# Kernel optimization log

Hardware: AMD Instinct MI355X
Metric: run time of the kernel (lower is better)

The kernel has to match this reference:

```python
import jax, jax.numpy as jnp
import numpy as np

B, H, S, D = 2, 16, 2048, 64

def setup_inputs() -> dict:
    key = jax.random.key(0)
    kq, kk, kv = jax.random.split(key, 3)
    query = jax.random.normal(kq, (B, H, S, D), dtype=jnp.float32)
    k = jax.random.normal(kk, (B, H, S, D), dtype=jnp.float32)
    value = jax.random.normal(kv, (B, H, S, D), dtype=jnp.float32)
    return {"query": query, "key": k, "value": value}

def reference(query, key, value):
    d_k = query.shape[-1]
    scale = 1.0 / jnp.sqrt(jnp.asarray(d_k, dtype=jnp.float32))
    # scores: [B, H, S, S]
    scores = jnp.einsum('bhqd,bhkd->bhqk', query, key) * scale
    attn = jax.nn.softmax(scores, axis=-1)
    # output: [B, H, S, D]
    return jnp.einsum('bhqk,bhkd->bhqd', attn, value)
```

## Files before the change

kernel.cpp:

```cpp
#include <hip/hip_runtime.h>
#include <hip/hip_bf16.h>

#define S_LEN 2048
#define HD    64
#define BH    32
#define QB    16
#define KVB   64
#define NIT   (S_LEN / KVB)
#define ELEMS_PER_ARR (BH * S_LEN * HD)

typedef __attribute__((ext_vector_type(8))) short bf16x8;
typedef __attribute__((ext_vector_type(4))) float f32x4;

union FragU { unsigned u[4]; bf16x8 v; };

__device__ __forceinline__ unsigned cvtpk(float lo, float hi) {
  unsigned r;
  asm("v_cvt_pk_bf16_f32 %0, %1, %2" : "=v"(r) : "v"(lo), "v"(hi));
  return r;
}

__device__ __forceinline__ f32x4 mfma16(bf16x8 a, bf16x8 b, f32x4 c) {
  return __builtin_amdgcn_mfma_f32_16x16x32_bf16(a, b, c, 0, 0, 0);
}

__global__ __launch_bounds__(256) void cvt_qk(
    const float* __restrict__ Q, const float* __restrict__ K,
    unsigned short* __restrict__ Qb, unsigned short* __restrict__ Kb) {
  const int which = blockIdx.x >> 11;
  const size_t i = ((size_t)(blockIdx.x & 2047) * 256 + threadIdx.x) * 8;
  const float* src = which ? K : Q;
  unsigned short* dst = which ? Kb : Qb;
  const float sc = which ? 1.0f : (0.125f * 1.44269504088896340736f);
  float4 a = *(const float4*)(src + i);
  float4 b = *(const float4*)(src + i + 4);
  uint4 w;
  w.x = cvtpk(a.x * sc, a.y * sc);
  w.y = cvtpk(a.z * sc, a.w * sc);
  w.z = cvtpk(b.x * sc, b.y * sc);
  w.w = cvtpk(b.z * sc, b.w * sc);
  *(uint4*)(dst + i) = w;
}

__global__ __launch_bounds__(256) void transpose_v(
    const float* __restrict__ V, unsigned short* __restrict__ Vt) {
  __shared__ float T[64 * 68];
  const int tid = threadIdx.x;
  const int bh = blockIdx.x >> 5;
  const int s0 = (blockIdx.x & 31) * 64;
  const float* vb = V + ((size_t)bh * S_LEN + s0) * HD;
  {
    const int r = tid >> 4, c4 = (tid & 15) * 4;
#pragma unroll
    for (int i = 0; i < 4; ++i) {
      float4 x = *(const float4*)(vb + (size_t)(r + 16 * i) * HD + c4);
      *(float4*)&T[(r + 16 * i) * 68 + c4] = x;
    }
  }
  __syncthreads();
  const int d = tid >> 2, sc = (tid & 3) * 16;
  unsigned short* out = Vt + (size_t)bh * HD * S_LEN + (size_t)d * S_LEN + s0 + sc;
  uint4 w0, w1;
  w0.x = cvtpk(T[(sc + 0) * 68 + d], T[(sc + 1) * 68 + d]);
  w0.y = cvtpk(T[(sc + 2) * 68 + d], T[(sc + 3) * 68 + d]);
  w0.z = cvtpk(T[(sc + 4) * 68 + d], T[(sc + 5) * 68 + d]);
  w0.w = cvtpk(T[(sc + 6) * 68 + d], T[(sc + 7) * 68 + d]);
  w1.x = cvtpk(T[(sc + 8) * 68 + d], T[(sc + 9) * 68 + d]);
  w1.y = cvtpk(T[(sc + 10) * 68 + d], T[(sc + 11) * 68 + d]);
  w1.z = cvtpk(T[(sc + 12) * 68 + d], T[(sc + 13) * 68 + d]);
  w1.w = cvtpk(T[(sc + 14) * 68 + d], T[(sc + 15) * 68 + d]);
  *(uint4*)out = w0;
  *(uint4*)(out + 8) = w1;
}

__device__ __forceinline__ void redist(const f32x4& pa, const f32x4& pc,
                                       int srcA, unsigned sel, FragU& pb) {
  unsigned pk0 = cvtpk(pa[0], pc[0]);
  unsigned pk1 = cvtpk(pa[1], pc[1]);
  unsigned pk2 = cvtpk(pa[2], pc[2]);
  unsigned pk3 = cvtpk(pa[3], pc[3]);
  unsigned w0 = (unsigned)__shfl((int)pk0, srcA);
  unsigned w1 = (unsigned)__shfl((int)pk1, srcA);
  unsigned w2 = (unsigned)__shfl((int)pk2, srcA);
  unsigned w3 = (unsigned)__shfl((int)pk3, srcA);
  unsigned w4 = (unsigned)__shfl((int)pk0, srcA + 16);
  unsigned w5 = (unsigned)__shfl((int)pk1, srcA + 16);
  unsigned w6 = (unsigned)__shfl((int)pk2, srcA + 16);
  unsigned w7 = (unsigned)__shfl((int)pk3, srcA + 16);
  pb.u[0] = __builtin_amdgcn_perm(w1, w0, sel);
  pb.u[1] = __builtin_amdgcn_perm(w3, w2, sel);
  pb.u[2] = __builtin_amdgcn_perm(w5, w4, sel);
  pb.u[3] = __builtin_amdgcn_perm(w7, w6, sel);
}

__global__ __launch_bounds__(256) void sdpa_main(
    const unsigned short* __restrict__ Qb, const unsigned short* __restrict__ Kb,
    const unsigned short* __restrict__ Vt, float* __restrict__ O) {
  __shared__ __align__(16) unsigned short Klds[2][KVB * 64];
  __shared__ __align__(16) unsigned short Vlds[2][HD * KVB];

  const int tid  = threadIdx.x;
  const int lane = tid & 63;
  const int wv   = tid >> 6;
  const int g    = lane >> 4;
  const int q15  = lane & 15;
  const int q7   = q15 & 7;

  const int bh   = blockIdx.x >> 5;
  const int qblk = blockIdx.x & 31;
  const int qt   = qblk * 64 + wv * QB;

  const unsigned short* Qp = Qb + (size_t)bh * S_LEN * HD;
  const unsigned short* Kp = Kb + (size_t)bh * S_LEN * HD;
  const unsigned short* Vp = Vt + (size_t)bh * HD * S_LEN;
  float* Op = O + (size_t)bh * S_LEN * HD;

  FragU qf0, qf1;
  qf0.v = *(const bf16x8*)(Qp + (size_t)(qt + q15) * HD + 8 * g);
  qf1.v = *(const bf16x8*)(Qp + (size_t)(qt + q15) * HD + 32 + 8 * g);

  const int rk = tid >> 2;
  const int qq = (tid & 3) * 16;
  const int r7 = rk & 7;
  const int wb0 = rk * 64 + (((qq >> 3)) ^ r7) * 8;
  const int wb1 = rk * 64 + (((qq >> 3) | 1) ^ r7) * 8;

  const int      srcA = 32 * (g & 1) + q15;
  const unsigned sel  = (g >= 2) ? 0x07060302u : 0x05040100u;

  bf16x8 sK0 = *(const bf16x8*)(Kp + (size_t)rk * HD + qq);
  bf16x8 sK1 = *(const bf16x8*)(Kp + (size_t)rk * HD + qq + 8);
  bf16x8 sV0 = *(const bf16x8*)(Vp + (size_t)rk * S_LEN + qq);
  bf16x8 sV1 = *(const bf16x8*)(Vp + (size_t)rk * S_LEN + qq + 8);
  *(bf16x8*)&Klds[0][wb0] = sK0;
  *(bf16x8*)&Klds[0][wb1] = sK1;
  *(bf16x8*)&Vlds[0][wb0] = sV0;
  *(bf16x8*)&Vlds[0][wb1] = sV1;
  __syncthreads();

  f32x4 acc0 = {0.f, 0.f, 0.f, 0.f};
  f32x4 acc1 = acc0, acc2 = acc0, acc3 = acc0;
  float m = -__builtin_inff();
  float l = 0.f;
  int cur = 0;

  for (int it = 0; it < NIT; ++it) {
    const bool more = (it + 1) < NIT;
    const int ktn = (it + 1) * KVB;
    if (more) {
      sK0 = *(const bf16x8*)(Kp + (size_t)(ktn + rk) * HD + qq);
      sK1 = *(const bf16x8*)(Kp + (size_t)(ktn + rk) * HD + qq + 8);
      sV0 = *(const bf16x8*)(Vp + (size_t)rk * S_LEN + ktn + qq);
      sV1 = *(const bf16x8*)(Vp + (size_t)rk * S_LEN + ktn + qq + 8);
    }
    const bf16x8* K8 = (const bf16x8*)&Klds[cur][0];
    const bf16x8* V8 = (const bf16x8*)&Vlds[cur][0];

    f32x4 st0 = {0.f, 0.f, 0.f, 0.f}, st1 = st0, st2 = st0, st3 = st0;
    {
      bf16x8 ka, kb;
      ka = K8[(q15) * 8 + (g ^ q7)];
      kb = K8[(q15) * 8 + ((g ^ 4) ^ q7)];
      st0 = mfma16(ka, qf0.v, st0); st0 = mfma16(kb, qf1.v, st0);
      ka = K8[(16 + q15) * 8 + (g ^ q7)];
      kb = K8[(16 + q15) * 8 + ((g ^ 4) ^ q7)];
      st1 = mfma16(ka, qf0.v, st1); st1 = mfma16(kb, qf1.v, st1);
      ka = K8[(32 + q15) * 8 + (g ^ q7)];
      kb = K8[(32 + q15) * 8 + ((g ^ 4) ^ q7)];
      st2 = mfma16(ka, qf0.v, st2); st2 = mfma16(kb, qf1.v, st2);
      ka = K8[(48 + q15) * 8 + (g ^ q7)];
      kb = K8[(48 + q15) * 8 + ((g ^ 4) ^ q7)];
      st3 = mfma16(ka, qf0.v, st3); st3 = mfma16(kb, qf1.v, st3);
    }

    float tm = fmaxf(fmaxf(fmaxf(st0[0], st0[1]), fmaxf(st0[2], st0[3])),
                     fmaxf(fmaxf(st1[0], st1[1]), fmaxf(st1[2], st1[3])));
    tm = fmaxf(tm, fmaxf(fmaxf(fmaxf(st2[0], st2[1]), fmaxf(st2[2], st2[3])),
                         fmaxf(fmaxf(st3[0], st3[1]), fmaxf(st3[2], st3[3]))));
    tm = fmaxf(tm, __shfl_xor(tm, 16));
    tm = fmaxf(tm, __shfl_xor(tm, 32));
    const float mn    = fmaxf(m, tm);
    const float alpha = __builtin_amdgcn_exp2f(m - mn);
    m = mn;

    float rs = 0.f;
#pragma unroll
    for (int r = 0; r < 4; ++r) {
      st0[r] = __builtin_amdgcn_exp2f(st0[r] - mn);
      st1[r] = __builtin_amdgcn_exp2f(st1[r] - mn);
      st2[r] = __builtin_amdgcn_exp2f(st2[r] - mn);
      st3[r] = __builtin_amdgcn_exp2f(st3[r] - mn);
      rs += (st0[r] + st1[r]) + (st2[r] + st3[r]);
    }
    rs += __shfl_xor(rs, 16);
    rs += __shfl_xor(rs, 32);
    l = l * alpha + rs;
    acc0 *= alpha; acc1 *= alpha; acc2 *= alpha; acc3 *= alpha;

    FragU pb0, pb1;
    redist(st0, st1, srcA, sel, pb0);
    redist(st2, st3, srcA, sel, pb1);

    {
      bf16x8 va, vb;
      va = V8[(q15) * 8 + (g ^ q7)];
      vb = V8[(q15) * 8 + ((g ^ 4) ^ q7)];
      acc0 = mfma16(va, pb0.v, acc0); acc0 = mfma16(vb, pb1.v, acc0);
      va = V8[(16 + q15) * 8 + (g ^ q7)];
      vb = V8[(16 + q15) * 8 + ((g ^ 4) ^ q7)];
      acc1 = mfma16(va, pb0.v, acc1); acc1 = mfma16(vb, pb1.v, acc1);
      va = V8[(32 + q15) * 8 + (g ^ q7)];
      vb = V8[(32 + q15) * 8 + ((g ^ 4) ^ q7)];
      acc2 = mfma16(va, pb0.v, acc2); acc2 = mfma16(vb, pb1.v, acc2);
      va = V8[(48 + q15) * 8 + (g ^ q7)];
      vb = V8[(48 + q15) * 8 + ((g ^ 4) ^ q7)];
      acc3 = mfma16(va, pb0.v, acc3); acc3 = mfma16(vb, pb1.v, acc3);
    }

    if (more) {
      *(bf16x8*)&Klds[cur ^ 1][wb0] = sK0;
      *(bf16x8*)&Klds[cur ^ 1][wb1] = sK1;
      *(bf16x8*)&Vlds[cur ^ 1][wb0] = sV0;
      *(bf16x8*)&Vlds[cur ^ 1][wb1] = sV1;
    }
    __syncthreads();
    cur ^= 1;
  }

  const float inv = 1.0f / l;
  float* orow = Op + (size_t)(qt + q15) * HD + 4 * g;
  float4 o;
  o.x = acc0[0] * inv; o.y = acc0[1] * inv; o.z = acc0[2] * inv; o.w = acc0[3] * inv;
  *(float4*)(orow + 0) = o;
  o.x = acc1[0] * inv; o.y = acc1[1] * inv; o.z = acc1[2] * inv; o.w = acc1[3] * inv;
  *(float4*)(orow + 16) = o;
  o.x = acc2[0] * inv; o.y = acc2[1] * inv; o.z = acc2[2] * inv; o.w = acc2[3] * inv;
  *(float4*)(orow + 32) = o;
  o.x = acc3[0] * inv; o.y = acc3[1] * inv; o.z = acc3[2] * inv; o.w = acc3[3] * inv;
  *(float4*)(orow + 48) = o;
}

#define KROW 72
#define VROW 40
__global__ __launch_bounds__(256) void sdpa_fallback(
    const float* __restrict__ Q, const float* __restrict__ K,
    const float* __restrict__ V, float* __restrict__ O) {
  __shared__ __align__(16) unsigned short Klds[32 * KROW];
  __shared__ __align__(16) unsigned short Vlds[HD * VROW];
  const int tid = threadIdx.x;
  const int lane = tid & 63;
  const int wv = tid >> 6;
  const int g = lane >> 4;
  const int q15 = lane & 15;
  const int bh = blockIdx.x >> 5;
  const int qblk = blockIdx.x & 31;
  const int qt = qblk * 64 + wv * QB;
  const size_t base = (size_t)bh * S_LEN * HD;
  const float* Qp = Q + base;
  const float* Kp = K + base;
  const float* Vp = V + base;
  float* Op = O + base;
  const float qs = 0.125f * 1.44269504088896340736f;
  FragU qf0, qf1;
  {
    const float* qrow = Qp + (size_t)(qt + q15) * HD + 8 * g;
    float4 a = *(const float4*)(qrow);
    float4 b = *(const float4*)(qrow + 4);
    qf0.u[0] = cvtpk(a.x * qs, a.y * qs); qf0.u[1] = cvtpk(a.z * qs, a.w * qs);
    qf0.u[2] = cvtpk(b.x * qs, b.y * qs); qf0.u[3] = cvtpk(b.z * qs, b.w * qs);
    a = *(const float4*)(qrow + 32);
    b = *(const float4*)(qrow + 36);
    qf1.u[0] = cvtpk(a.x * qs, a.y * qs); qf1.u[1] = cvtpk(a.z * qs, a.w * qs);
    qf1.u[2] = cvtpk(b.x * qs, b.y * qs); qf1.u[3] = cvtpk(b.z * qs, b.w * qs);
  }
  f32x4 acc0 = {0.f,0.f,0.f,0.f};
  f32x4 acc1 = acc0, acc2 = acc0, acc3 = acc0;
  float m = -__builtin_inff();
  float l = 0.f;
  const int srcA = 32 * (g & 1) + q15;
  const unsigned sel = (g >= 2) ? 0x07060302u : 0x05040100u;
  const int sk = tid >> 3;
  const int sd = (tid & 7) * 8;
  const bf16x8* Kv = (const bf16x8*)Klds;
  const bf16x8* Vv = (const bf16x8*)Vlds;
  for (int kt = 0; kt < S_LEN; kt += 32) {
    __syncthreads();
    {
      const float* p = Kp + (size_t)(kt + sk) * HD + sd;
      float4 a = *(const float4*)p;
      float4 b = *(const float4*)(p + 4);
      uint4 w;
      w.x = cvtpk(a.x, a.y); w.y = cvtpk(a.z, a.w);
      w.z = cvtpk(b.x, b.y); w.w = cvtpk(b.z, b.w);
      *(uint4*)&Klds[sk * KROW + sd] = w;
    }
    {
      const float* p = Vp + (size_t)(kt + sk) * HD + sd;
      float4 a = *(const float4*)p;
      float4 b = *(const float4*)(p + 4);
      unsigned u0 = cvtpk(a.x, a.y), u1 = cvtpk(a.z, a.w);
      unsigned u2 = cvtpk(b.x, b.y), u3 = cvtpk(b.z, b.w);
      Vlds[(sd + 0) * VROW + sk] = (unsigned short)(u0 & 0xffffu);
      Vlds[(sd + 1) * VROW + sk] = (unsigned short)(u0 >> 16);
      Vlds[(sd + 2) * VROW + sk] = (unsigned short)(u1 & 0xffffu);
      Vlds[(sd + 3) * VROW + sk] = (unsigned short)(u1 >> 16);
      Vlds[(sd + 4) * VROW + sk] = (unsigned short)(u2 & 0xffffu);
      Vlds[(sd + 5) * VROW + sk] = (unsigned short)(u2 >> 16);
      Vlds[(sd + 6) * VROW + sk] = (unsigned short)(u3 & 0xffffu);
      Vlds[(sd + 7) * VROW + sk] = (unsigned short)(u3 >> 16);
    }
    __syncthreads();
    f32x4 st0 = {0.f,0.f,0.f,0.f}, st1 = st0;
    {
      bf16x8 kfa = Kv[q15 * 9 + g];
      bf16x8 kfb = Kv[q15 * 9 + 4 + g];
      st0 = mfma16(kfa, qf0.v, st0);
      st0 = mfma16(kfb, qf1.v, st0);
      bf16x8 kfc = Kv[(16 + q15) * 9 + g];
      bf16x8 kfd = Kv[(16 + q15) * 9 + 4 + g];
      st1 = mfma16(kfc, qf0.v, st1);
      st1 = mfma16(kfd, qf1.v, st1);
    }
    float tm = fmaxf(fmaxf(fmaxf(st0[0], st0[1]), fmaxf(st0[2], st0[3])),
                     fmaxf(fmaxf(st1[0], st1[1]), fmaxf(st1[2], st1[3])));
    tm = fmaxf(tm, __shfl_xor(tm, 16));
    tm = fmaxf(tm, __shfl_xor(tm, 32));
    const float mn = fmaxf(m, tm);
    const float alpha = __builtin_amdgcn_exp2f(m - mn);
    m = mn;
    float rs = 0.f;
#pragma unroll
    for (int r = 0; r < 4; ++r) {
      st0[r] = __builtin_amdgcn_exp2f(st0[r] - mn);
      st1[r] = __builtin_amdgcn_exp2f(st1[r] - mn);
      rs += st0[r] + st1[r];
    }
    rs += __shfl_xor(rs, 16);
    rs += __shfl_xor(rs, 32);
    l = l * alpha + rs;
    acc0 *= alpha; acc1 *= alpha; acc2 *= alpha; acc3 *= alpha;
    FragU pb;
    redist(st0, st1, srcA, sel, pb);
    {
      bf16x8 vf0 = Vv[q15 * 5 + g];
      bf16x8 vf1 = Vv[(16 + q15) * 5 + g];
      bf16x8 vf2 = Vv[(32 + q15) * 5 + g];
      bf16x8 vf3 = Vv[(48 + q15) * 5 + g];
      acc0 = mfma16(vf0, pb.v, acc0);
      acc1 = mfma16(vf1, pb.v, acc1);
      acc2 = mfma16(vf2, pb.v, acc2);
      acc3 = mfma16(vf3, pb.v, acc3);
    }
  }
  const float inv = 1.0f / l;
  float* orow = Op + (size_t)(qt + q15) * HD + 4 * g;
  float4 o;
  o.x = acc0[0]*inv; o.y = acc0[1]*inv; o.z = acc0[2]*inv; o.w = acc0[3]*inv;
  *(float4*)(orow +  0) = o;
  o.x = acc1[0]*inv; o.y = acc1[1]*inv; o.z = acc1[2]*inv; o.w = acc1[3]*inv;
  *(float4*)(orow + 16) = o;
  o.x = acc2[0]*inv; o.y = acc2[1]*inv; o.z = acc2[2]*inv; o.w = acc2[3]*inv;
  *(float4*)(orow + 32) = o;
  o.x = acc3[0]*inv; o.y = acc3[1]*inv; o.z = acc3[2]*inv; o.w = acc3[3]*inv;
  *(float4*)(orow + 48) = o;
}

extern "C" void kernel_launch(void* const* d_in, const int* in_sizes, int n_in,
                              void* d_out, int out_size, void* d_ws, size_t ws_size,
                              hipStream_t stream) {
  const float* Q = (const float*)d_in[0];
  const float* K = (const float*)d_in[1];
  const float* V = (const float*)d_in[2];
  float* O = (float*)d_out;
  const size_t need = (size_t)3 * ELEMS_PER_ARR * 2;
  if (ws_size >= need) {
    unsigned short* Qb = (unsigned short*)d_ws;
    unsigned short* Kb = Qb + ELEMS_PER_ARR;
    unsigned short* Vt = Kb + ELEMS_PER_ARR;
    cvt_qk<<<4096, 256, 0, stream>>>(Q, K, Qb, Kb);
    transpose_v<<<1024, 256, 0, stream>>>(V, Vt);
    sdpa_main<<<1024, 256, 0, stream>>>(Qb, Kb, Vt, O);
  } else {
    sdpa_fallback<<<1024, 256, 0, stream>>>(Q, K, V, O);
  }
}
```

Baseline: 165.5 us.

## Switch attention to 32x32 MFMA tiles with lazy rescaling and fused Q conversion

Replaces the 16x16 MFMA attention kernel with one using 32x32x16 bf16 MFMAs, giving each wave 32 query rows and each block 128 queries. The softmax probabilities are repacked with v_permlane32_swap instead of shuffle-based redistribution. Rescaling of the running max is skipped unless the new max exceeds the old one by more than 8 in log2 units. The change also adds s_setprio around the MFMA sections, XCD-aware block remapping, and moves Q conversion into the main kernel, which drops the separate Q pass. The trade-off is higher register pressure from the 16-wide accumulators and half as many blocks.

New measurement: 142.5 us. -13.8%, faster.

```diff
diff --git a/kernel.cpp b/kernel.cpp
--- a/kernel.cpp
+++ b/kernel.cpp
@@ -4,13 +4,13 @@
 #define S_LEN 2048
 #define HD    64
 #define BH    32
-#define QB    16
 #define KVB   64
 #define NIT   (S_LEN / KVB)
 #define ELEMS_PER_ARR (BH * S_LEN * HD)
 
-typedef __attribute__((ext_vector_type(8))) short bf16x8;
-typedef __attribute__((ext_vector_type(4))) float f32x4;
+typedef __attribute__((ext_vector_type(8)))  short bf16x8;
+typedef __attribute__((ext_vector_type(4)))  float f32x4;
+typedef __attribute__((ext_vector_type(16))) float f32x16;
 
 union FragU { unsigned u[4]; bf16x8 v; };
 
@@ -23,23 +23,30 @@
 __device__ __forceinline__ f32x4 mfma16(bf16x8 a, bf16x8 b, f32x4 c) {
   return __builtin_amdgcn_mfma_f32_16x16x32_bf16(a, b, c, 0, 0, 0);
 }
-
-__global__ __launch_bounds__(256) void cvt_qk(
-    const float* __restrict__ Q, const float* __restrict__ K,
-    unsigned short* __restrict__ Qb, unsigned short* __restrict__ Kb) {
-  const int which = blockIdx.x >> 11;
-  const size_t i = ((size_t)(blockIdx.x & 2047) * 256 + threadIdx.x) * 8;
-  const float* src = which ? K : Q;
-  unsigned short* dst = which ? Kb : Qb;
-  const float sc = which ? 1.0f : (0.125f * 1.44269504088896340736f);
-  float4 a = *(const float4*)(src + i);
-  float4 b = *(const float4*)(src + i + 4);
+__device__ __forceinline__ f32x16 mfma32(bf16x8 a, bf16x8 b, f32x16 c) {
+  return __builtin_amdgcn_mfma_f32_32x32x16_bf16(a, b, c, 0, 0, 0);
+}
+
+template <int B>
+__device__ __forceinline__ void pack_chunk(const f32x16& s, FragU& p) {
+  unsigned wA = cvtpk(s[B + 0], s[B + 1]);
+  unsigned wB = cvtpk(s[B + 2], s[B + 3]);
+  unsigned wC = cvtpk(s[B + 4], s[B + 5]);
+  unsigned wD = cvtpk(s[B + 6], s[B + 7]);
+  asm("v_permlane32_swap_b32 %0, %1" : "+v"(wA), "+v"(wC));
+  asm("v_permlane32_swap_b32 %0, %1" : "+v"(wB), "+v"(wD));
+  p.u[0] = wA; p.u[1] = wB; p.u[2] = wC; p.u[3] = wD;
+}
+
+__global__ __launch_bounds__(256) void cvt_k(
+    const float* __restrict__ K, unsigned short* __restrict__ Kb) {
+  const size_t i = ((size_t)blockIdx.x * 256 + threadIdx.x) * 8;
+  float4 a = *(const float4*)(K + i);
+  float4 b = *(const float4*)(K + i + 4);
   uint4 w;
-  w.x = cvtpk(a.x * sc, a.y * sc);
-  w.y = cvtpk(a.z * sc, a.w * sc);
-  w.z = cvtpk(b.x * sc, b.y * sc);
-  w.w = cvtpk(b.z * sc, b.w * sc);
-  *(uint4*)(dst + i) = w;
+  w.x = cvtpk(a.x, a.y); w.y = cvtpk(a.z, a.w);
+  w.z = cvtpk(b.x, b.y); w.w = cvtpk(b.z, b.w);
+  *(uint4*)(Kb + i) = w;
 }
 
 __global__ __launch_bounds__(256) void transpose_v(
@@ -73,6 +80,173 @@
   *(uint4*)(out + 8) = w1;
 }
 
+__global__ __launch_bounds__(256, 2) void sdpa_main32(
+    const float* __restrict__ Q, const unsigned short* __restrict__ Kb,
+    const unsigned short* __restrict__ Vt, float* __restrict__ O) {
+  __shared__ __align__(16) unsigned short Klds[2][KVB * 64];
+  __shared__ __align__(16) unsigned short Vlds[2][HD * KVB];
+
+  const int tid  = threadIdx.x;
+  const int lane = tid & 63;
+  const int wv   = tid >> 6;
+  const int q31  = lane & 31;
+  const int hi   = lane >> 5;
+  const int r7   = q31 & 7;
+
+  const int bid  = blockIdx.x;
+  const int obid = (bid & 7) * 64 + (bid >> 3);
+  const int bh   = obid >> 4;
+  const int qblk = obid & 15;
+  const int q0   = qblk * 128 + wv * 32;
+
+  const float* Qp = Q + (size_t)bh * S_LEN * HD;
+  const unsigned short* Kp = Kb + (size_t)bh * S_LEN * HD;
+  const unsigned short* Vp = Vt + (size_t)bh * HD * S_LEN;
+  float* Op = O + (size_t)bh * S_LEN * HD;
+
+  const float qs = 0.125f * 1.44269504088896340736f;
+  FragU qb[4];
+  {
+    const float* qrow = Qp + (size_t)(q0 + q31) * HD + 8 * hi;
+#pragma unroll
+    for (int dc = 0; dc < 4; ++dc) {
+      float4 a = *(const float4*)(qrow + dc * 16);
+      float4 b = *(const float4*)(qrow + dc * 16 + 4);
+      qb[dc].u[0] = cvtpk(a.x * qs, a.y * qs);
+      qb[dc].u[1] = cvtpk(a.z * qs, a.w * qs);
+      qb[dc].u[2] = cvtpk(b.x * qs, b.y * qs);
+      qb[dc].u[3] = cvtpk(b.z * qs, b.w * qs);
+    }
+  }
+
+  const int rk  = tid >> 2;
+  const int qq  = (tid & 3) * 16;
+  const int rr7 = rk & 7;
+  const int wb0 = rk * 64 + (((qq >> 3)) ^ rr7) * 8;
+  const int wb1 = rk * 64 + (((qq >> 3) | 1) ^ rr7) * 8;
+
+  bf16x8 sK0 = *(const bf16x8*)(Kp + (size_t)rk * HD + qq);
+  bf16x8 sK1 = *(const bf16x8*)(Kp + (size_t)rk * HD + qq + 8);
+  bf16x8 sV0 = *(const bf16x8*)(Vp + (size_t)rk * S_LEN + qq);
+  bf16x8 sV1 = *(const bf16x8*)(Vp + (size_t)rk * S_LEN + qq + 8);
+  *(bf16x8*)&Klds[0][wb0] = sK0;
+  *(bf16x8*)&Klds[0][wb1] = sK1;
+  *(bf16x8*)&Vlds[0][wb0] = sV0;
+  *(bf16x8*)&Vlds[0][wb1] = sV1;
+  __syncthreads();
+
+  const f32x16 z16 = {0,0,0,0, 0,0,0,0, 0,0,0,0, 0,0,0,0};
+  f32x16 acc0 = z16, acc1 = z16;
+  float m = -__builtin_inff();
+  float l = 0.f;
+  int cur = 0;
+
+  for (int it = 0; it < NIT; ++it) {
+    const bool more = (it + 1) < NIT;
+    const int ktn = (it + 1) * KVB;
+    if (more) {
+      sK0 = *(const bf16x8*)(Kp + (size_t)(ktn + rk) * HD + qq);
+      sK1 = *(const bf16x8*)(Kp + (size_t)(ktn + rk) * HD + qq + 8);
+      sV0 = *(const bf16x8*)(Vp + (size_t)rk * S_LEN + ktn + qq);
+      sV1 = *(const bf16x8*)(Vp + (size_t)rk * S_LEN + ktn + qq + 8);
+    }
+    const bf16x8* K8 = (const bf16x8*)&Klds[cur][0];
+    const bf16x8* V8 = (const bf16x8*)&Vlds[cur][0];
+
+    f32x16 st0 = z16, st1 = z16;
+    __builtin_amdgcn_s_setprio(1);
+#pragma unroll
+    for (int dc = 0; dc < 4; ++dc) {
+      const int slot = (2 * dc + hi) ^ r7;
+      bf16x8 ka0 = K8[q31 * 8 + slot];
+      bf16x8 ka1 = K8[(32 + q31) * 8 + slot];
+      st0 = mfma32(ka0, qb[dc].v, st0);
+      st1 = mfma32(ka1, qb[dc].v, st1);
+    }
+    __builtin_amdgcn_s_setprio(0);
+
+    float tm = fmaxf(
+        fmaxf(fmaxf(fmaxf(st0[0], st0[1]), fmaxf(st0[2], st0[3])),
+              fmaxf(fmaxf(st0[4], st0[5]), fmaxf(st0[6], st0[7]))),
+        fmaxf(fmaxf(fmaxf(st0[8], st0[9]), fmaxf(st0[10], st0[11])),
+              fmaxf(fmaxf(st0[12], st0[13]), fmaxf(st0[14], st0[15]))));
+    tm = fmaxf(tm, fmaxf(
+        fmaxf(fmaxf(fmaxf(st1[0], st1[1]), fmaxf(st1[2], st1[3])),
+              fmaxf(fmaxf(st1[4], st1[5]), fmaxf(st1[6], st1[7]))),
+        fmaxf(fmaxf(fmaxf(st1[8], st1[9]), fmaxf(st1[10], st1[11])),
+              fmaxf(fmaxf(st1[12], st1[13]), fmaxf(st1[14], st1[15])))));
+    tm = fmaxf(tm, __shfl_xor(tm, 32));
+
+    if (__any(tm > m + 8.0f)) {
+      const float mn = fmaxf(m, tm);
+      const float alpha = __builtin_amdgcn_exp2f(m - mn);
+      m = mn;
+      l *= alpha;
+      acc0 *= alpha;
+      acc1 *= alpha;
+    }
+
+    float rs = 0.f;
+#pragma unroll
+    for (int j = 0; j < 16; ++j) {
+      st0[j] = __builtin_amdgcn_exp2f(st0[j] - m);
+      rs += st0[j];
+    }
+#pragma unroll
+    for (int j = 0; j < 16; ++j) {
+      st1[j] = __builtin_amdgcn_exp2f(st1[j] - m);
+      rs += st1[j];
+    }
+    rs += __shfl_xor(rs, 32);
+    l += rs;
+
+    FragU pb[4];
+    pack_chunk<0>(st0, pb[0]);
+    pack_chunk<8>(st0, pb[1]);
+    pack_chunk<0>(st1, pb[2]);
+    pack_chunk<8>(st1, pb[3]);
+
+    __builtin_amdgcn_s_setprio(1);
+#pragma unroll
+    for (int c = 0; c < 4; ++c) {
+      const int slot = (2 * c + hi) ^ r7;
+      bf16x8 va0 = V8[q31 * 8 + slot];
+      bf16x8 va1 = V8[(32 + q31) * 8 + slot];
+      acc0 = mfma32(va0, pb[c].v, acc0);
+      acc1 = mfma32(va1, pb[c].v, acc1);
+    }
+    __builtin_amdgcn_s_setprio(0);
+
+    if (more) {
+      *(bf16x8*)&Klds[cur ^ 1][wb0] = sK0;
+      *(bf16x8*)&Klds[cur ^ 1][wb1] = sK1;
+      *(bf16x8*)&Vlds[cur ^ 1][wb0] = sV0;
+      *(bf16x8*)&Vlds[cur ^ 1][wb1] = sV1;
+    }
+    __syncthreads();
+    cur ^= 1;
+  }
+
+  const float inv = 1.0f / l;
+  float* orow = Op + (size_t)(q0 + q31) * HD + 4 * hi;
+#pragma unroll
+  for (int u = 0; u < 4; ++u) {
+    float4 o;
+    o.x = acc0[4 * u + 0] * inv; o.y = acc0[4 * u + 1] * inv;
+    o.z = acc0[4 * u + 2] * inv; o.w = acc0[4 * u + 3] * inv;
+    *(float4*)(orow + 8 * u) = o;
+  }
+#pragma unroll
+  for (int u = 0; u < 4; ++u) {
+    float4 o;
+    o.x = acc1[4 * u + 0] * inv; o.y = acc1[4 * u + 1] * inv;
+    o.z = acc1[4 * u + 2] * inv; o.w = acc1[4 * u + 3] * inv;
+    *(float4*)(orow + 32 + 8 * u) = o;
+  }
+}
+
+#define KROW 72
+#define VROW 40
 __device__ __forceinline__ void redist(const f32x4& pa, const f32x4& pc,
                                        int srcA, unsigned sel, FragU& pb) {
   unsigned pk0 = cvtpk(pa[0], pc[0]);
@@ -93,155 +267,6 @@
   pb.u[3] = __builtin_amdgcn_perm(w7, w6, sel);
 }
 
-__global__ __launch_bounds__(256) void sdpa_main(
-    const unsigned short* __restrict__ Qb, const unsigned short* __restrict__ Kb,
-    const unsigned short* __restrict__ Vt, float* __restrict__ O) {
-  __shared__ __align__(16) unsigned short Klds[2][KVB * 64];
-  __shared__ __align__(16) unsigned short Vlds[2][HD * KVB];
-
-  const int tid  = threadIdx.x;
-  const int lane = tid & 63;
-  const int wv   = tid >> 6;
-  const int g    = lane >> 4;
-  const int q15  = lane & 15;
-  const int q7   = q15 & 7;
-
-  const int bh   = blockIdx.x >> 5;
-  const int qblk = blockIdx.x & 31;
-  const int qt   = qblk * 64 + wv * QB;
-
-  const unsigned short* Qp = Qb + (size_t)bh * S_LEN * HD;
-  const unsigned short* Kp = Kb + (size_t)bh * S_LEN * HD;
-  const unsigned short* Vp = Vt + (size_t)bh * HD * S_LEN;
-  float* Op = O + (size_t)bh * S_LEN * HD;
-
-  FragU qf0, qf1;
-  qf0.v = *(const bf16x8*)(Qp + (size_t)(qt + q15) * HD + 8 * g);
-  qf1.v = *(const bf16x8*)(Qp + (size_t)(qt + q15) * HD + 32 + 8 * g);
-
-  const int rk = tid >> 2;
-  const int qq = (tid & 3) * 16;
-  const int r7 = rk & 7;
-  const int wb0 = rk * 64 + (((qq >> 3)) ^ r7) * 8;
-  const int wb1 = rk * 64 + (((qq >> 3) | 1) ^ r7) * 8;
-
-  const int      srcA = 32 * (g & 1) + q15;
-  const unsigned sel  = (g >= 2) ? 0x07060302u : 0x05040100u;
-
-  bf16x8 sK0 = *(const bf16x8*)(Kp + (size_t)rk * HD + qq);
-  bf16x8 sK1 = *(const bf16x8*)(Kp + (size_t)rk * HD + qq + 8);
-  bf16x8 sV0 = *(const bf16x8*)(Vp + (size_t)rk * S_LEN + qq);
-  bf16x8 sV1 = *(const bf16x8*)(Vp + (size_t)rk * S_LEN + qq + 8);
-  *(bf16x8*)&Klds[0][wb0] = sK0;
-  *(bf16x8*)&Klds[0][wb1] = sK1;
-  *(bf16x8*)&Vlds[0][wb0] = sV0;
-  *(bf16x8*)&Vlds[0][wb1] = sV1;
-  __syncthreads();
-
-  f32x4 acc0 = {0.f, 0.f, 0.f, 0.f};
-  f32x4 acc1 = acc0, acc2 = acc0, acc3 = acc0;
-  float m = -__builtin_inff();
-  float l = 0.f;
-  int cur = 0;
-
-  for (int it = 0; it < NIT; ++it) {
-    const bool more = (it + 1) < NIT;
-    const int ktn = (it + 1) * KVB;
-    if (more) {
-      sK0 = *(const bf16x8*)(Kp + (size_t)(ktn + rk) * HD + qq);
-      sK1 = *(const bf16x8*)(Kp + (size_t)(ktn + rk) * HD + qq + 8);
-      sV0 = *(const bf16x8*)(Vp + (size_t)rk * S_LEN + ktn + qq);
-      sV1 = *(const bf16x8*)(Vp + (size_t)rk * S_LEN + ktn + qq + 8);
-    }
-    const bf16x8* K8 = (const bf16x8*)&Klds[cur][0];
-    const bf16x8* V8 = (const bf16x8*)&Vlds[cur][0];
-
-    f32x4 st0 = {0.f, 0.f, 0.f, 0.f}, st1 = st0, st2 = st0, st3 = st0;
-    {
-      bf16x8 ka, kb;
-      ka = K8[(q15) * 8 + (g ^ q7)];
-      kb = K8[(q15) * 8 + ((g ^ 4) ^ q7)];
-      st0 = mfma16(ka, qf0.v, st0); st0 = mfma16(kb, qf1.v, st0);
-      ka = K8[(16 + q15) * 8 + (g ^ q7)];
-      kb = K8[(16 + q15) * 8 + ((g ^ 4) ^ q7)];
-      st1 = mfma16(ka, qf0.v, st1); st1 = mfma16(kb, qf1.v, st1);
-      ka = K8[(32 + q15) * 8 + (g ^ q7)];
-      kb = K8[(32 + q15) * 8 + ((g ^ 4) ^ q7)];
-      st2 = mfma16(ka, qf0.v, st2); st2 = mfma16(kb, qf1.v, st2);
-      ka = K8[(48 + q15) * 8 + (g ^ q7)];
-      kb = K8[(48 + q15) * 8 + ((g ^ 4) ^ q7)];
-      st3 = mfma16(ka, qf0.v, st3); st3 = mfma16(kb, qf1.v, st3);
-    }
-
-    float tm = fmaxf(fmaxf(fmaxf(st0[0], st0[1]), fmaxf(st0[2], st0[3])),
-                     fmaxf(fmaxf(st1[0], st1[1]), fmaxf(st1[2], st1[3])));
-    tm = fmaxf(tm, fmaxf(fmaxf(fmaxf(st2[0], st2[1]), fmaxf(st2[2], st2[3])),
-                         fmaxf(fmaxf(st3[0], st3[1]), fmaxf(st3[2], st3[3]))));
-    tm = fmaxf(tm, __shfl_xor(tm, 16));
-    tm = fmaxf(tm, __shfl_xor(tm, 32));
-    const float mn    = fmaxf(m, tm);
-    const float alpha = __builtin_amdgcn_exp2f(m - mn);
-    m = mn;
-
-    float rs = 0.f;
-#pragma unroll
-    for (int r = 0; r < 4; ++r) {
-      st0[r] = __builtin_amdgcn_exp2f(st0[r] - mn);
-      st1[r] = __builtin_amdgcn_exp2f(st1[r] - mn);
-      st2[r] = __builtin_amdgcn_exp2f(st2[r] - mn);
-      st3[r] = __builtin_amdgcn_exp2f(st3[r] - mn);
-      rs += (st0[r] + st1[r]) + (st2[r] + st3[r]);
-    }
-    rs += __shfl_xor(rs, 16);
-    rs += __shfl_xor(rs, 32);
-    l = l * alpha + rs;
-    acc0 *= alpha; acc1 *= alpha; acc2 *= alpha; acc3 *= alpha;
-
-    FragU pb0, pb1;
-    redist(st0, st1, srcA, sel, pb0);
-    redist(st2, st3, srcA, sel, pb1);
-
-    {
-      bf16x8 va, vb;
-      va = V8[(q15) * 8 + (g ^ q7)];
-      vb = V8[(q15) * 8 + ((g ^ 4) ^ q7)];
-      acc0 = mfma16(va, pb0.v, acc0); acc0 = mfma16(vb, pb1.v, acc0);
-      va = V8[(16 + q15) * 8 + (g ^ q7)];
-      vb = V8[(16 + q15) * 8 + ((g ^ 4) ^ q7)];
-      acc1 = mfma16(va, pb0.v, acc1); acc1 = mfma16(vb, pb1.v, acc1);
-      va = V8[(32 + q15) * 8 + (g ^ q7)];
-      vb = V8[(32 + q15) * 8 + ((g ^ 4) ^ q7)];
-      acc2 = mfma16(va, pb0.v, acc2); acc2 = mfma16(vb, pb1.v, acc2);
-      va = V8[(48 + q15) * 8 + (g ^ q7)];
-      vb = V8[(48 + q15) * 8 + ((g ^ 4) ^ q7)];
-      acc3 = mfma16(va, pb0.v, acc3); acc3 = mfma16(vb, pb1.v, acc3);
-    }
-
-    if (more) {
-      *(bf16x8*)&Klds[cur ^ 1][wb0] = sK0;
-      *(bf16x8*)&Klds[cur ^ 1][wb1] = sK1;
-      *(bf16x8*)&Vlds[cur ^ 1][wb0] = sV0;
-      *(bf16x8*)&Vlds[cur ^ 1][wb1] = sV1;
-    }
-    __syncthreads();
-    cur ^= 1;
-  }
-
-  const float inv = 1.0f / l;
-  float* orow = Op + (size_t)(qt + q15) * HD + 4 * g;
-  float4 o;
-  o.x = acc0[0] * inv; o.y = acc0[1] * inv; o.z = acc0[2] * inv; o.w = acc0[3] * inv;
-  *(float4*)(orow + 0) = o;
-  o.x = acc1[0] * inv; o.y = acc1[1] * inv; o.z = acc1[2] * inv; o.w = acc1[3] * inv;
-  *(float4*)(orow + 16) = o;
-  o.x = acc2[0] * inv; o.y = acc2[1] * inv; o.z = acc2[2] * inv; o.w = acc2[3] * inv;
-  *(float4*)(orow + 32) = o;
-  o.x = acc3[0] * inv; o.y = acc3[1] * inv; o.z = acc3[2] * inv; o.w = acc3[3] * inv;
-  *(float4*)(orow + 48) = o;
-}
-
-#define KROW 72
-#define VROW 40
 __global__ __launch_bounds__(256) void sdpa_fallback(
     const float* __restrict__ Q, const float* __restrict__ K,
     const float* __restrict__ V, float* __restrict__ O) {
@@ -254,7 +279,7 @@
   const int q15 = lane & 15;
   const int bh = blockIdx.x >> 5;
   const int qblk = blockIdx.x & 31;
-  const int qt = qblk * 64 + wv * QB;
+  const int qt = qblk * 64 + wv * 16;
   const size_t base = (size_t)bh * S_LEN * HD;
   const float* Qp = Q + base;
   const float* Kp = K + base;
@@ -372,14 +397,13 @@
   const float* K = (const float*)d_in[1];
   const float* V = (const float*)d_in[2];
   float* O = (float*)d_out;
-  const size_t need = (size_t)3 * ELEMS_PER_ARR * 2;
+  const size_t need = (size_t)2 * ELEMS_PER_ARR * 2;
   if (ws_size >= need) {
-    unsigned short* Qb = (unsigned short*)d_ws;
-    unsigned short* Kb = Qb + ELEMS_PER_ARR;
+    unsigned short* Kb = (unsigned short*)d_ws;
     unsigned short* Vt = Kb + ELEMS_PER_ARR;
-    cvt_qk<<<4096, 256, 0, stream>>>(Q, K, Qb, Kb);
+    cvt_k<<<2048, 256, 0, stream>>>(K, Kb);
     transpose_v<<<1024, 256, 0, stream>>>(V, Vt);
-    sdpa_main<<<1024, 256, 0, stream>>>(Qb, Kb, Vt, O);
+    sdpa_main32<<<512, 256, 0, stream>>>(Q, Kb, Vt, O);
   } else {
     sdpa_fallback<<<1024, 256, 0, stream>>>(Q, K, V, O);
   }
```
